# Kernel tuning notes

Hardware: AMD Instinct MI355X
Metric: run time of the kernel (lower is better)

The kernel has to match this reference:

```python
import jax, jax.numpy as jnp
import numpy as np

NUM_HEADS = 12

def setup_inputs() -> dict:
    key = jax.random.key(0)
    k1, k2, k3 = jax.random.split(key, 3)
    B, T, C = 1, 4096, 768
    x = jax.random.normal(k1, (B, T, C), dtype=jnp.float32)
    w_qkv = jax.random.normal(k2, (3 * C, C), dtype=jnp.float32) * (1.0 / np.sqrt(C))
    w_proj = jax.random.normal(k3, (C, C), dtype=jnp.float32) * (1.0 / np.sqrt(C))
    attn_mask = jnp.tril(jnp.ones((T, T), dtype=bool))  # causal block mask
    return {"x": x, "w_qkv": w_qkv, "w_proj": w_proj, "attn_mask": attn_mask}


def reference(x, w_qkv, w_proj, attn_mask):
    B, T, C = x.shape
    H = NUM_HEADS
    Dh = C // H
    # fused QKV projection (torch Linear: y = x @ W.T), then split
    qkv = jnp.einsum('btc,fc->btf', x, w_qkv)  # [B,T,3C]
    q, k, v = jnp.split(qkv, 3, axis=-1)
    # [B,T,C] -> [B,H,T,Dh]
    q = q.reshape(B, T, H, Dh).transpose(0, 2, 1, 3)
    k = k.reshape(B, T, H, Dh).transpose(0, 2, 1, 3)
    v = v.reshape(B, T, H, Dh).transpose(0, 2, 1, 3)
    # masked SDPA, default flex_attention scale = 1/sqrt(head_dim)
    scores = jnp.einsum('bhqd,bhkd->bhqk', q, k) * (1.0 / np.sqrt(Dh))
    neg = jnp.finfo(scores.dtype).min
    scores = jnp.where(attn_mask[None, None, :, :], scores, neg)
    attn = jax.nn.softmax(scores, axis=-1)
    y = jnp.einsum('bhqk,bhkd->bhqd', attn, v)
    # [B,H,T,Dh] -> [B,T,C], then output projection (dropout=0)
    y = y.transpose(0, 2, 1, 3).reshape(B, T, C)
    y = jnp.einsum('btc,fc->btf', y, w_proj)
    return y
```

## Files before the change

### kernel.cpp

```cpp
#include <hip/hip_runtime.h>

typedef unsigned short u16;
typedef unsigned int u32;
typedef __attribute__((ext_vector_type(8))) short s16x8;
typedef __attribute__((ext_vector_type(4))) float f32x4;
typedef __attribute__((ext_vector_type(4))) u16 u16x4;
typedef __attribute__((ext_vector_type(4))) u32 u32x4;

#define LOG2E 1.4426950408889634f

#if __has_builtin(__builtin_amdgcn_exp2f)
#define EXP2F __builtin_amdgcn_exp2f
#else
#define EXP2F exp2f
#endif

__device__ __forceinline__ u16 f32_to_bf16(float f) {
  union { float f; u32 u; } c; c.f = f;
  return (u16)((c.u + 0x7fffu + ((c.u >> 16) & 1u)) >> 16);
}

__device__ __forceinline__ u32 cvtpk(float lo, float hi) {
  u32 r;
  asm("v_cvt_pk_bf16_f32 %0, %1, %2" : "=v"(r) : "v"(lo), "v"(hi));
  return r;
}

__device__ __forceinline__ void async16(const void* g, void* l) {
  __builtin_amdgcn_global_load_lds(
      (__attribute__((address_space(1))) void*)g,
      (__attribute__((address_space(3))) void*)l, 16, 0, 0);
}

__global__ __launch_bounds__(256) void cast3_f32_bf16(const float* __restrict__ a,
                                                      const float* __restrict__ b,
                                                      const float* __restrict__ c,
                                                      u16* __restrict__ out,
                                                      int n1, int n2, int n3) {
  int i = (blockIdx.x * 256 + threadIdx.x) * 4;
  const float* src;
  int off = i;
  if (i < n1) {
    src = a;
  } else if (i < n1 + n2) {
    src = b; off = i - n1;
  } else if (i < n1 + n2 + n3) {
    src = c; off = i - n1 - n2;
  } else {
    return;
  }
  f32x4 v = *(const f32x4*)(src + off);
  u16x4 o;
  o[0] = f32_to_bf16(v[0]);
  o[1] = f32_to_bf16(v[1]);
  o[2] = f32_to_bf16(v[2]);
  o[3] = f32_to_bf16(v[3]);
  *(u16x4*)(out + i) = o;
}

__device__ __forceinline__ int vt_perm_inv(int k) {
  return (k & 35) | ((k & 16) >> 2) | ((k & 12) << 1);
}

__global__ __launch_bounds__(512) void qkv_gemm(const u16* __restrict__ A,
                                                const u16* __restrict__ B,
                                                u16* __restrict__ qk,
                                                u16* __restrict__ vt) {
  constexpr int K = 768;
  constexpr int BK = 32;
  constexpr int NT = K / BK;
  __shared__ alignas(16) u16 As[2][128 * BK];
  __shared__ alignas(16) u16 Bs[2][128 * BK];
  const int tid = threadIdx.x;
  const int lane = tid & 63;
  const int wid = tid >> 6;
  const int brow = blockIdx.x * 128;
  const int bcol = blockIdx.y * 128;
  const int wr = wid >> 2, wc = wid & 3;
  const int l15 = lane & 15, l4 = lane >> 4;
  f32x4 acc[4][2] = {};
  const int r0 = tid >> 2, s0 = tid & 3;

#define G1_STAGE(kt, b)                                                         \
  {                                                                             \
    async16(A + (size_t)(brow + r0) * K + (kt) * BK + s0 * 8, &As[b][tid * 8]); \
    async16(B + (size_t)(bcol + r0) * K + (kt) * BK + s0 * 8, &Bs[b][tid * 8]); \
  }

  G1_STAGE(0, 0);
  __syncthreads();
  int cur = 0;
  for (int kt = 0; kt < NT; ++kt) {
    if (kt + 1 < NT) G1_STAGE(kt + 1, cur ^ 1);
    s16x8 af[4], bf[2];
#pragma unroll
    for (int m = 0; m < 4; ++m)
      af[m] = *(const s16x8*)&As[cur][(wr * 64 + m * 16 + l15) * BK + l4 * 8];
#pragma unroll
    for (int n = 0; n < 2; ++n)
      bf[n] = *(const s16x8*)&Bs[cur][(wc * 32 + n * 16 + l15) * BK + l4 * 8];
#pragma unroll
    for (int m = 0; m < 4; ++m)
#pragma unroll
      for (int n = 0; n < 2; ++n)
        acc[m][n] = __builtin_amdgcn_mfma_f32_16x16x32_bf16(af[m], bf[n], acc[m][n], 0, 0, 0);
    __syncthreads();
    cur ^= 1;
  }
#undef G1_STAGE

  const int row0 = brow + wr * 64 + l4 * 4;
  const int col0 = bcol + wc * 32 + l15;
  if (bcol >= 1536) {
#pragma unroll
    for (int m = 0; m < 4; ++m) {
      int t0 = row0 + m * 16;
      int s = (t0 & ~63) + vt_perm_inv(t0 & 63);
#pragma unroll
      for (int n = 0; n < 2; ++n) {
        int vcol = col0 + n * 16 - 1536;
        u16x4 pk;
#pragma unroll
        for (int r = 0; r < 4; ++r) pk[r] = f32_to_bf16(acc[m][n][r]);
        *(u16x4*)&vt[(size_t)vcol * 4096 + s] = pk;
      }
    }
  } else {
    const float qs = (bcol < 768) ? 0.125f * LOG2E : 1.0f;
#pragma unroll
    for (int m = 0; m < 4; ++m)
#pragma unroll
      for (int n = 0; n < 2; ++n)
#pragma unroll
        for (int r = 0; r < 4; ++r)
          qk[(size_t)(row0 + m * 16 + r) * 1536 + (col0 + n * 16)] =
              f32_to_bf16(acc[m][n][r] * qs);
  }
}

__global__ __launch_bounds__(512) void proj_gemm(const u16* __restrict__ A,
                                                 const u16* __restrict__ B,
                                                 float* __restrict__ C) {
  constexpr int K = 768;
  constexpr int N = 768;
  constexpr int BK = 32;
  constexpr int NT = K / BK;
  __shared__ alignas(16) u16 As[2][128 * BK];
  __shared__ alignas(16) u16 Bs[2][128 * BK];
  const int tid = threadIdx.x;
  const int lane = tid & 63;
  const int wid = tid >> 6;
  const int brow = blockIdx.x * 128;
  const int bcol = blockIdx.y * 128;
  const int wr = wid >> 2, wc = wid & 3;
  const int l15 = lane & 15, l4 = lane >> 4;
  f32x4 acc[4][2] = {};
  const int r0 = tid >> 2, s0 = tid & 3;

#define G2_STAGE(kt, b)                                                         \
  {                                                                             \
    async16(A + (size_t)(brow + r0) * K + (kt) * BK + s0 * 8, &As[b][tid * 8]); \
    async16(B + (size_t)(bcol + r0) * K + (kt) * BK + s0 * 8, &Bs[b][tid * 8]); \
  }

  G2_STAGE(0, 0);
  __syncthreads();
  int cur = 0;
  for (int kt = 0; kt < NT; ++kt) {
    if (kt + 1 < NT) G2_STAGE(kt + 1, cur ^ 1);
    s16x8 af[4], bf[2];
#pragma unroll
    for (int m = 0; m < 4; ++m)
      af[m] = *(const s16x8*)&As[cur][(wr * 64 + m * 16 + l15) * BK + l4 * 8];
#pragma unroll
    for (int n = 0; n < 2; ++n)
      bf[n] = *(const s16x8*)&Bs[cur][(wc * 32 + n * 16 + l15) * BK + l4 * 8];
#pragma unroll
    for (int m = 0; m < 4; ++m)
#pragma unroll
      for (int n = 0; n < 2; ++n)
        acc[m][n] = __builtin_amdgcn_mfma_f32_16x16x32_bf16(af[m], bf[n], acc[m][n], 0, 0, 0);
    __syncthreads();
    cur ^= 1;
  }
#undef G2_STAGE

  const int row0 = brow + wr * 64 + l4 * 4;
  const int col0 = bcol + wc * 32 + l15;
#pragma unroll
  for (int m = 0; m < 4; ++m)
#pragma unroll
    for (int n = 0; n < 2; ++n)
#pragma unroll
      for (int r = 0; r < 4; ++r)
        C[(size_t)(row0 + m * 16 + r) * N + (col0 + n * 16)] = acc[m][n][r];
}

constexpr int cph_for(int C) {
  int s = 0;
  for (int qb = 0; qb < 32; ++qb) s += (2 * qb + 2 + C - 1) / C;
  return s;
}

template <int C>
__global__ __launch_bounds__(256) void attn_kernel(const u16* __restrict__ qk,
                                                   const u16* __restrict__ vt,
                                                   u16* __restrict__ y,
                                                   float* __restrict__ po,
                                                   float* __restrict__ pl) {
  constexpr int MAXCH = (64 + C - 1) / C;
  constexpr int CPH = cph_for(C);
  __shared__ alignas(16) u16 Ks[2][64 * 64];
  __shared__ alignas(16) u16 Vs[2][64 * 64];
  const int tid = threadIdx.x;
  const int lane = tid & 63;
  const int wid = tid >> 6;
  const int l15 = lane & 15, l4 = lane >> 4;

  const int h = blockIdx.x % 12;
  int c = CPH - 1 - (int)(blockIdx.x / 12);
  int qb = 0, ch = c;
  for (;;) {
    int n = (2 * qb + 2 + C - 1) / C;
    if (ch < n) break;
    ch -= n;
    ++qb;
  }
  const int NTt = 2 * qb + 2;
  const int nch = (NTt + C - 1) / C;

  const int qw0 = qb * 128 + wid * 32;

  s16x8 bq[2][2];
#pragma unroll
  for (int qf = 0; qf < 2; ++qf)
#pragma unroll
    for (int ks = 0; ks < 2; ++ks)
      bq[qf][ks] = *(const s16x8*)&qk[(size_t)(qw0 + qf * 16 + l15) * 1536 +
                                      h * 64 + ks * 32 + l4 * 8];

  f32x4 o[2][4] = {};
  f32x4 lacc[2] = {};

  const u16* Kb = qk + 768 + h * 64;
  const u16* Vb = vt + (size_t)(h * 64) * 4096;

  const int sc0 = tid, sc1 = tid + 256;
  const int sr0 = sc0 >> 3, sp0 = sc0 & 7;
  const int sr1 = sc1 >> 3, sp1 = sc1 & 7;

#define STAGE_KV(t, b)                                                                        \
  {                                                                                           \
    async16(Kb + (size_t)((t) * 64 + sr0) * 1536 + ((sp0 ^ (sr0 & 7)) * 8), &Ks[b][sc0 * 8]); \
    async16(Kb + (size_t)((t) * 64 + sr1) * 1536 + ((sp1 ^ (sr1 & 7)) * 8), &Ks[b][sc1 * 8]); \
    async16(Vb + (size_t)sr0 * 4096 + (t) * 64 + ((sp0 ^ (sr0 & 7)) * 8), &Vs[b][sc0 * 8]);   \
    async16(Vb + (size_t)sr1 * 4096 + (t) * 64 + ((sp1 ^ (sr1 & 7)) * 8), &Vs[b][sc1 * 8]);   \
  }

  const int t0 = ch * C;
  const int t1 = (t0 + C < NTt) ? t0 + C : NTt;
  STAGE_KV(t0, 0);
  __syncthreads();
  int cur = 0;
  for (int kt = t0; kt < t1; ++kt) {
    if (kt + 1 < t1) STAGE_KV(kt + 1, cur ^ 1);

    f32x4 s4[2][4];
    __builtin_amdgcn_s_setprio(1);
#pragma unroll
    for (int kf = 0; kf < 4; ++kf) {
      int r = kf * 16 + l15;
      s16x8 k0 = *(const s16x8*)&Ks[cur][r * 64 + ((l4 ^ (r & 7)) * 8)];
      s16x8 k1 = *(const s16x8*)&Ks[cur][r * 64 + (((l4 + 4) ^ (r & 7)) * 8)];
#pragma unroll
      for (int qf = 0; qf < 2; ++qf) {
        f32x4 a = {};
        a = __builtin_amdgcn_mfma_f32_16x16x32_bf16(k0, bq[qf][0], a, 0, 0, 0);
        a = __builtin_amdgcn_mfma_f32_16x16x32_bf16(k1, bq[qf][1], a, 0, 0, 0);
        s4[qf][kf] = a;
      }
    }
    __builtin_amdgcn_s_setprio(0);
    if (kt >= 2 * qb) {
#pragma unroll
      for (int qf = 0; qf < 2; ++qf) {
        int qg = qw0 + qf * 16 + l15;
#pragma unroll
        for (int kf = 0; kf < 4; ++kf)
#pragma unroll
          for (int r = 0; r < 4; ++r)
            if (kt * 64 + kf * 16 + l4 * 4 + r > qg) s4[qf][kf][r] = -1e30f;
      }
    }
    u32 w[2][4][2];
#pragma unroll
    for (int qf = 0; qf < 2; ++qf)
#pragma unroll
      for (int kf = 0; kf < 4; ++kf) {
        f32x4 p;
#pragma unroll
        for (int r = 0; r < 4; ++r) p[r] = EXP2F(s4[qf][kf][r]);
        lacc[qf] += p;
        w[qf][kf][0] = cvtpk(p[0], p[1]);
        w[qf][kf][1] = cvtpk(p[2], p[3]);
      }
    __builtin_amdgcn_s_setprio(1);
#pragma unroll
    for (int ks2 = 0; ks2 < 2; ++ks2) {
      s16x8 bp[2];
#pragma unroll
      for (int qf = 0; qf < 2; ++qf) {
        u32x4 bu;
        bu[0] = w[qf][2 * ks2][0];
        bu[1] = w[qf][2 * ks2][1];
        bu[2] = w[qf][2 * ks2 + 1][0];
        bu[3] = w[qf][2 * ks2 + 1][1];
        bp[qf] = __builtin_bit_cast(s16x8, bu);
      }
#pragma unroll
      for (int df = 0; df < 4; ++df) {
        int d = df * 16 + l15;
        int e = ks2 * 4 + l4;
        s16x8 av = *(const s16x8*)&Vs[cur][d * 64 + ((e ^ (d & 7)) * 8)];
#pragma unroll
        for (int qf = 0; qf < 2; ++qf)
          o[qf][df] = __builtin_amdgcn_mfma_f32_16x16x32_bf16(av, bp[qf], o[qf][df], 0, 0, 0);
      }
    }
    __builtin_amdgcn_s_setprio(0);
    __syncthreads();
    cur ^= 1;
  }
#undef STAGE_KV

  float lsum[2];
#pragma unroll
  for (int qf = 0; qf < 2; ++qf) {
    float s = lacc[qf][0] + lacc[qf][1] + lacc[qf][2] + lacc[qf][3];
    s += __shfl_xor(s, 16);
    s += __shfl_xor(s, 32);
    lsum[qf] = s;
  }

  if (nch == 1) {
#pragma unroll
    for (int qf = 0; qf < 2; ++qf) {
      float inv = 1.0f / lsum[qf];
#pragma unroll
      for (int df = 0; df < 4; ++df) {
        u16x4 pk;
#pragma unroll
        for (int r = 0; r < 4; ++r) pk[r] = f32_to_bf16(o[qf][df][r] * inv);
        *(u16x4*)&y[(size_t)(qw0 + qf * 16 + l15) * 768 + h * 64 + df * 16 + l4 * 4] = pk;
      }
    }
  } else {
    const size_t slot = (size_t)(h * 32 + qb) * MAXCH + ch;
#pragma unroll
    for (int qf = 0; qf < 2; ++qf) {
      float* ob = po + slot * 8192 + (size_t)(wid * 32 + qf * 16 + l15) * 64;
#pragma unroll
      for (int df = 0; df < 4; ++df)
        *(f32x4*)(ob + df * 16 + l4 * 4) = o[qf][df];
      if (lane < 16) pl[slot * 128 + wid * 32 + qf * 16 + l15] = lsum[qf];
    }
  }
}

template <int C>
__global__ __launch_bounds__(256) void attn_combine(const float* __restrict__ po,
                                                    const float* __restrict__ pl,
                                                    u16* __restrict__ y) {
  constexpr int MAXCH = (64 + C - 1) / C;
  const int h = blockIdx.x;
  const int qb = C / 2 + blockIdx.y;
  const int nch = (2 * qb + 2 + C - 1) / C;
  const int tid = threadIdx.x;
  const int q = tid >> 1;
  const int d0 = (tid & 1) * 32;

  f32x4 acc[8] = {};
  float lt = 0.f;
  for (int s = 0; s < nch; ++s) {
    const size_t slot = (size_t)(h * 32 + qb) * MAXCH + s;
    lt += pl[slot * 128 + q];
    const float* ob = po + slot * 8192 + (size_t)q * 64 + d0;
#pragma unroll
    for (int j = 0; j < 8; ++j) acc[j] += *(const f32x4*)(ob + j * 4);
  }
  float inv = 1.0f / lt;
  u16* yp = &y[(size_t)(qb * 128 + q) * 768 + h * 64 + d0];
#pragma unroll
  for (int j = 0; j < 8; ++j) {
    u16x4 pk;
#pragma unroll
    for (int r = 0; r < 4; ++r) pk[r] = f32_to_bf16(acc[j][r] * inv);
    *(u16x4*)(yp + j * 4) = pk;
  }
}

extern "C" void kernel_launch(void* const* d_in, const int* in_sizes, int n_in,
                              void* d_out, int out_size, void* d_ws, size_t ws_size,
                              hipStream_t stream) {
  const float* x = (const float*)d_in[0];
  const float* w_qkv = (const float*)d_in[1];
  const float* w_proj = (const float*)d_in[2];
  float* out = (float*)d_out;

  u16* ws = (u16*)d_ws;
  u16* xb = ws;
  u16* wqkvb = xb + 4096 * 768;
  u16* wprojb = wqkvb + 2304 * 768;
  u16* qkb = wprojb + 768 * 768;
  u16* vtb = qkb + (size_t)4096 * 1536;
  u16* yb = vtb + (size_t)768 * 4096;
  const size_t base_u16 = (size_t)4096 * 768 + 2304 * 768 + 768 * 768 +
                          (size_t)4096 * 1536 + (size_t)768 * 4096 + (size_t)4096 * 768;
  float* pf = (float*)(ws + base_u16);
  const size_t base_b = base_u16 * 2;

  constexpr int N1 = 4096 * 768, N2 = 2304 * 768, N3 = 768 * 768;
  cast3_f32_bf16<<<(N1 + N2 + N3) / 4 / 256, 256, 0, stream>>>(
      x, w_qkv, w_proj, xb, N1, N2, N3);

  qkv_gemm<<<dim3(32, 18), 512, 0, stream>>>(xb, wqkvb, qkb, vtb);

  const size_t need8 = base_b + (size_t)(12 * 32 * 8) * (8192 + 128) * 4;
  const size_t need16 = base_b + (size_t)(12 * 32 * 4) * (8192 + 128) * 4;
  const size_t need32 = base_b + (size_t)(12 * 32 * 2) * (8192 + 128) * 4;
  if (ws_size >= need8) {
    constexpr int C = 8, MAXCH = 8;
    float* po = pf;
    float* pl = po + (size_t)12 * 32 * MAXCH * 8192;
    attn_kernel<C><<<12 * cph_for(C), 256, 0, stream>>>(qkb, vtb, yb, po, pl);
    attn_combine<C><<<dim3(12, 32 - C / 2), 256, 0, stream>>>(po, pl, yb);
  } else if (ws_size >= need16) {
    constexpr int C = 16, MAXCH = 4;
    float* po = pf;
    float* pl = po + (size_t)12 * 32 * MAXCH * 8192;
    attn_kernel<C><<<12 * cph_for(C), 256, 0, stream>>>(qkb, vtb, yb, po, pl);
    attn_combine<C><<<dim3(12, 32 - C / 2), 256, 0, stream>>>(po, pl, yb);
  } else if (ws_size >= need32) {
    constexpr int C = 32, MAXCH = 2;
    float* po = pf;
    float* pl = po + (size_t)12 * 32 * MAXCH * 8192;
    attn_kernel<C><<<12 * cph_for(C), 256, 0, stream>>>(qkb, vtb, yb, po, pl);
    attn_combine<C><<<dim3(12, 32 - C / 2), 256, 0, stream>>>(po, pl, yb);
  } else {
    constexpr int C = 64;
    attn_kernel<C><<<12 * cph_for(C), 256, 0, stream>>>(qkb, vtb, yb, nullptr, nullptr);
  }

  proj_gemm<<<dim3(32, 6), 512, 0, stream>>>(yb, wprojb, out);
}
```

Baseline: 114.3 us.

## Retile QKV and projection GEMMs and balance attention KV split chunks

Doubles the QKV GEMM K-tile to 64, adding an XOR swizzle on LDS to avoid bank conflicts. Shrinks the projection GEMM to 64x64 tiles with 256 threads so more blocks cover the device. Replaces the fixed-size attention KV chunking with a target-based even split, so chunk counts scale with each query block's causal length and the combine pass skips unsplit blocks. These aim to raise occupancy and balance work, at the cost of more LDS per block in the QKV GEMM and extra combine launches.

```diff
diff --git a/kernel.cpp b/kernel.cpp
--- a/kernel.cpp
+++ b/kernel.cpp
@@ -67,7 +67,7 @@
                                                 u16* __restrict__ qk,
                                                 u16* __restrict__ vt) {
   constexpr int K = 768;
-  constexpr int BK = 32;
+  constexpr int BK = 64;
   constexpr int NT = K / BK;
   __shared__ alignas(16) u16 As[2][128 * BK];
   __shared__ alignas(16) u16 Bs[2][128 * BK];
@@ -79,12 +79,16 @@
   const int wr = wid >> 2, wc = wid & 3;
   const int l15 = lane & 15, l4 = lane >> 4;
   f32x4 acc[4][2] = {};
-  const int r0 = tid >> 2, s0 = tid & 3;
-
-#define G1_STAGE(kt, b)                                                         \
-  {                                                                             \
-    async16(A + (size_t)(brow + r0) * K + (kt) * BK + s0 * 8, &As[b][tid * 8]); \
-    async16(B + (size_t)(bcol + r0) * K + (kt) * BK + s0 * 8, &Bs[b][tid * 8]); \
+  const int c0 = tid, c1 = tid + 512;
+  const int r0 = c0 >> 3, p0 = c0 & 7;
+  const int r1 = c1 >> 3, p1 = c1 & 7;
+
+#define G1_STAGE(kt, b)                                                                       \
+  {                                                                                           \
+    async16(A + (size_t)(brow + r0) * K + (kt) * BK + ((p0 ^ (r0 & 7)) * 8), &As[b][c0 * 8]); \
+    async16(A + (size_t)(brow + r1) * K + (kt) * BK + ((p1 ^ (r1 & 7)) * 8), &As[b][c1 * 8]); \
+    async16(B + (size_t)(bcol + r0) * K + (kt) * BK + ((p0 ^ (r0 & 7)) * 8), &Bs[b][c0 * 8]); \
+    async16(B + (size_t)(bcol + r1) * K + (kt) * BK + ((p1 ^ (r1 & 7)) * 8), &Bs[b][c1 * 8]); \
   }
 
   G1_STAGE(0, 0);
@@ -92,18 +96,27 @@
   int cur = 0;
   for (int kt = 0; kt < NT; ++kt) {
     if (kt + 1 < NT) G1_STAGE(kt + 1, cur ^ 1);
-    s16x8 af[4], bf[2];
+    s16x8 af[2][4], bf[2][2];
+#pragma unroll
+    for (int kk = 0; kk < 2; ++kk) {
+#pragma unroll
+      for (int m = 0; m < 4; ++m) {
+        int r = wr * 64 + m * 16 + l15;
+        af[kk][m] = *(const s16x8*)&As[cur][r * BK + (((kk * 4 + l4) ^ (r & 7)) * 8)];
+      }
+#pragma unroll
+      for (int n = 0; n < 2; ++n) {
+        int r = wc * 32 + n * 16 + l15;
+        bf[kk][n] = *(const s16x8*)&Bs[cur][r * BK + (((kk * 4 + l4) ^ (r & 7)) * 8)];
+      }
+    }
 #pragma unroll
     for (int m = 0; m < 4; ++m)
-      af[m] = *(const s16x8*)&As[cur][(wr * 64 + m * 16 + l15) * BK + l4 * 8];
-#pragma unroll
-    for (int n = 0; n < 2; ++n)
-      bf[n] = *(const s16x8*)&Bs[cur][(wc * 32 + n * 16 + l15) * BK + l4 * 8];
-#pragma unroll
-    for (int m = 0; m < 4; ++m)
-#pragma unroll
-      for (int n = 0; n < 2; ++n)
-        acc[m][n] = __builtin_amdgcn_mfma_f32_16x16x32_bf16(af[m], bf[n], acc[m][n], 0, 0, 0);
+#pragma unroll
+      for (int n = 0; n < 2; ++n) {
+        acc[m][n] = __builtin_amdgcn_mfma_f32_16x16x32_bf16(af[0][m], bf[0][n], acc[m][n], 0, 0, 0);
+        acc[m][n] = __builtin_amdgcn_mfma_f32_16x16x32_bf16(af[1][m], bf[1][n], acc[m][n], 0, 0, 0);
+      }
     __syncthreads();
     cur ^= 1;
   }
@@ -138,23 +151,23 @@
   }
 }
 
-__global__ __launch_bounds__(512) void proj_gemm(const u16* __restrict__ A,
+__global__ __launch_bounds__(256) void proj_gemm(const u16* __restrict__ A,
                                                  const u16* __restrict__ B,
                                                  float* __restrict__ C) {
   constexpr int K = 768;
   constexpr int N = 768;
   constexpr int BK = 32;
   constexpr int NT = K / BK;
-  __shared__ alignas(16) u16 As[2][128 * BK];
-  __shared__ alignas(16) u16 Bs[2][128 * BK];
+  __shared__ alignas(16) u16 As[2][64 * BK];
+  __shared__ alignas(16) u16 Bs[2][64 * BK];
   const int tid = threadIdx.x;
   const int lane = tid & 63;
   const int wid = tid >> 6;
-  const int brow = blockIdx.x * 128;
-  const int bcol = blockIdx.y * 128;
-  const int wr = wid >> 2, wc = wid & 3;
+  const int brow = blockIdx.x * 64;
+  const int bcol = blockIdx.y * 64;
+  const int wr = wid >> 1, wc = wid & 1;
   const int l15 = lane & 15, l4 = lane >> 4;
-  f32x4 acc[4][2] = {};
+  f32x4 acc[2][2] = {};
   const int r0 = tid >> 2, s0 = tid & 3;
 
 #define G2_STAGE(kt, b)                                                         \
@@ -168,15 +181,15 @@
   int cur = 0;
   for (int kt = 0; kt < NT; ++kt) {
     if (kt + 1 < NT) G2_STAGE(kt + 1, cur ^ 1);
-    s16x8 af[4], bf[2];
-#pragma unroll
-    for (int m = 0; m < 4; ++m)
-      af[m] = *(const s16x8*)&As[cur][(wr * 64 + m * 16 + l15) * BK + l4 * 8];
+    s16x8 af[2], bf[2];
+#pragma unroll
+    for (int m = 0; m < 2; ++m)
+      af[m] = *(const s16x8*)&As[cur][(wr * 32 + m * 16 + l15) * BK + l4 * 8];
 #pragma unroll
     for (int n = 0; n < 2; ++n)
       bf[n] = *(const s16x8*)&Bs[cur][(wc * 32 + n * 16 + l15) * BK + l4 * 8];
 #pragma unroll
-    for (int m = 0; m < 4; ++m)
+    for (int m = 0; m < 2; ++m)
 #pragma unroll
       for (int n = 0; n < 2; ++n)
         acc[m][n] = __builtin_amdgcn_mfma_f32_16x16x32_bf16(af[m], bf[n], acc[m][n], 0, 0, 0);
@@ -185,10 +198,10 @@
   }
 #undef G2_STAGE
 
-  const int row0 = brow + wr * 64 + l4 * 4;
+  const int row0 = brow + wr * 32 + l4 * 4;
   const int col0 = bcol + wc * 32 + l15;
 #pragma unroll
-  for (int m = 0; m < 4; ++m)
+  for (int m = 0; m < 2; ++m)
 #pragma unroll
     for (int n = 0; n < 2; ++n)
 #pragma unroll
@@ -196,20 +209,23 @@
         C[(size_t)(row0 + m * 16 + r) * N + (col0 + n * 16)] = acc[m][n][r];
 }
 
-constexpr int cph_for(int C) {
+__host__ __device__ constexpr int nch_for(int qb, int TGT) {
+  int n = (2 * qb + 2 + TGT / 2 - 1) / TGT;
+  return n < 1 ? 1 : n;
+}
+__host__ __device__ constexpr int cph_for(int TGT) {
   int s = 0;
-  for (int qb = 0; qb < 32; ++qb) s += (2 * qb + 2 + C - 1) / C;
+  for (int qb = 0; qb < 32; ++qb) s += nch_for(qb, TGT);
   return s;
 }
 
-template <int C>
+template <int TGT, int MAXCH>
 __global__ __launch_bounds__(256) void attn_kernel(const u16* __restrict__ qk,
                                                    const u16* __restrict__ vt,
                                                    u16* __restrict__ y,
                                                    float* __restrict__ po,
                                                    float* __restrict__ pl) {
-  constexpr int MAXCH = (64 + C - 1) / C;
-  constexpr int CPH = cph_for(C);
+  constexpr int CPH = cph_for(TGT);
   __shared__ alignas(16) u16 Ks[2][64 * 64];
   __shared__ alignas(16) u16 Vs[2][64 * 64];
   const int tid = threadIdx.x;
@@ -221,13 +237,13 @@
   int c = CPH - 1 - (int)(blockIdx.x / 12);
   int qb = 0, ch = c;
   for (;;) {
-    int n = (2 * qb + 2 + C - 1) / C;
+    int n = nch_for(qb, TGT);
     if (ch < n) break;
     ch -= n;
     ++qb;
   }
   const int NTt = 2 * qb + 2;
-  const int nch = (NTt + C - 1) / C;
+  const int nch = nch_for(qb, TGT);
 
   const int qw0 = qb * 128 + wid * 32;
 
@@ -257,8 +273,8 @@
     async16(Vb + (size_t)sr1 * 4096 + (t) * 64 + ((sp1 ^ (sr1 & 7)) * 8), &Vs[b][sc1 * 8]);   \
   }
 
-  const int t0 = ch * C;
-  const int t1 = (t0 + C < NTt) ? t0 + C : NTt;
+  const int t0 = ch * NTt / nch;
+  const int t1 = (ch + 1) * NTt / nch;
   STAGE_KV(t0, 0);
   __syncthreads();
   int cur = 0;
@@ -367,14 +383,14 @@
   }
 }
 
-template <int C>
+template <int TGT, int MAXCH>
 __global__ __launch_bounds__(256) void attn_combine(const float* __restrict__ po,
                                                     const float* __restrict__ pl,
                                                     u16* __restrict__ y) {
-  constexpr int MAXCH = (64 + C - 1) / C;
   const int h = blockIdx.x;
-  const int qb = C / 2 + blockIdx.y;
-  const int nch = (2 * qb + 2 + C - 1) / C;
+  const int qb = blockIdx.y;
+  const int nch = nch_for(qb, TGT);
+  if (nch == 1) return;
   const int tid = threadIdx.x;
   const int q = tid >> 1;
   const int d0 = (tid & 1) * 32;
@@ -425,31 +441,17 @@
 
   qkv_gemm<<<dim3(32, 18), 512, 0, stream>>>(xb, wqkvb, qkb, vtb);
 
-  const size_t need8 = base_b + (size_t)(12 * 32 * 8) * (8192 + 128) * 4;
-  const size_t need16 = base_b + (size_t)(12 * 32 * 4) * (8192 + 128) * 4;
-  const size_t need32 = base_b + (size_t)(12 * 32 * 2) * (8192 + 128) * 4;
-  if (ws_size >= need8) {
-    constexpr int C = 8, MAXCH = 8;
+  constexpr int TGT = 12;
+  constexpr int MAXCH = nch_for(31, TGT);
+  const size_t need = base_b + (size_t)(12 * 32 * MAXCH) * (8192 + 128) * 4;
+  if (ws_size >= need) {
     float* po = pf;
     float* pl = po + (size_t)12 * 32 * MAXCH * 8192;
-    attn_kernel<C><<<12 * cph_for(C), 256, 0, stream>>>(qkb, vtb, yb, po, pl);
-    attn_combine<C><<<dim3(12, 32 - C / 2), 256, 0, stream>>>(po, pl, yb);
-  } else if (ws_size >= need16) {
-    constexpr int C = 16, MAXCH = 4;
-    float* po = pf;
-    float* pl = po + (size_t)12 * 32 * MAXCH * 8192;
-    attn_kernel<C><<<12 * cph_for(C), 256, 0, stream>>>(qkb, vtb, yb, po, pl);
-    attn_combine<C><<<dim3(12, 32 - C / 2), 256, 0, stream>>>(po, pl, yb);
-  } else if (ws_size >= need32) {
-    constexpr int C = 32, MAXCH = 2;
-    float* po = pf;
-    float* pl = po + (size_t)12 * 32 * MAXCH * 8192;
-    attn_kernel<C><<<12 * cph_for(C), 256, 0, stream>>>(qkb, vtb, yb, po, pl);
-    attn_combine<C><<<dim3(12, 32 - C / 2), 256, 0, stream>>>(po, pl, yb);
+    attn_kernel<TGT, MAXCH><<<12 * cph_for(TGT), 256, 0, stream>>>(qkb, vtb, yb, po, pl);
+    attn_combine<TGT, MAXCH><<<dim3(12, 32), 256, 0, stream>>>(po, pl, yb);
   } else {
-    constexpr int C = 64;
-    attn_kernel<C><<<12 * cph_for(C), 256, 0, stream>>>(qkb, vtb, yb, nullptr, nullptr);
-  }
-
-  proj_gemm<<<dim3(32, 6), 512, 0, stream>>>(yb, wprojb, out);
-}
+    attn_kernel<1000, 1><<<12 * cph_for(1000), 256, 0, stream>>>(qkb, vtb, yb, nullptr, nullptr);
+  }
+
+  proj_gemm<<<dim3(64, 12), 256, 0, stream>>>(yb, wprojb, out);
+}
```

Result: no change. 114.3 us (+0.0%).

## Shrink proj tiles, single-buffer attention KV, compute row sums via MFMA

Applied to the files above, without the earlier changes.

The projection GEMM moves to 64x64 tiles with 256 threads and a 64x12 grid, giving more blocks for the CUs. The attention kernel drops KV double buffering in favour of one LDS buffer with two barriers per tile. This cuts LDS use and may allow more blocks per CU, but it loses the overlap of loads with compute. Softmax row sums are now computed with an extra MFMA against a ones vector instead of VALU adds and shuffles. The combine launch covers all query blocks and returns early for single-chunk ones.

```diff
diff --git a/kernel.cpp b/kernel.cpp
--- a/kernel.cpp
+++ b/kernel.cpp
@@ -138,23 +138,23 @@
   }
 }
 
-__global__ __launch_bounds__(512) void proj_gemm(const u16* __restrict__ A,
+__global__ __launch_bounds__(256) void proj_gemm(const u16* __restrict__ A,
                                                  const u16* __restrict__ B,
                                                  float* __restrict__ C) {
   constexpr int K = 768;
   constexpr int N = 768;
   constexpr int BK = 32;
   constexpr int NT = K / BK;
-  __shared__ alignas(16) u16 As[2][128 * BK];
-  __shared__ alignas(16) u16 Bs[2][128 * BK];
+  __shared__ alignas(16) u16 As[2][64 * BK];
+  __shared__ alignas(16) u16 Bs[2][64 * BK];
   const int tid = threadIdx.x;
   const int lane = tid & 63;
   const int wid = tid >> 6;
-  const int brow = blockIdx.x * 128;
-  const int bcol = blockIdx.y * 128;
-  const int wr = wid >> 2, wc = wid & 3;
+  const int brow = blockIdx.x * 64;
+  const int bcol = blockIdx.y * 64;
+  const int wr = wid >> 1, wc = wid & 1;
   const int l15 = lane & 15, l4 = lane >> 4;
-  f32x4 acc[4][2] = {};
+  f32x4 acc[2][2] = {};
   const int r0 = tid >> 2, s0 = tid & 3;
 
 #define G2_STAGE(kt, b)                                                         \
@@ -168,15 +168,15 @@
   int cur = 0;
   for (int kt = 0; kt < NT; ++kt) {
     if (kt + 1 < NT) G2_STAGE(kt + 1, cur ^ 1);
-    s16x8 af[4], bf[2];
-#pragma unroll
-    for (int m = 0; m < 4; ++m)
-      af[m] = *(const s16x8*)&As[cur][(wr * 64 + m * 16 + l15) * BK + l4 * 8];
+    s16x8 af[2], bf[2];
+#pragma unroll
+    for (int m = 0; m < 2; ++m)
+      af[m] = *(const s16x8*)&As[cur][(wr * 32 + m * 16 + l15) * BK + l4 * 8];
 #pragma unroll
     for (int n = 0; n < 2; ++n)
       bf[n] = *(const s16x8*)&Bs[cur][(wc * 32 + n * 16 + l15) * BK + l4 * 8];
 #pragma unroll
-    for (int m = 0; m < 4; ++m)
+    for (int m = 0; m < 2; ++m)
 #pragma unroll
       for (int n = 0; n < 2; ++n)
         acc[m][n] = __builtin_amdgcn_mfma_f32_16x16x32_bf16(af[m], bf[n], acc[m][n], 0, 0, 0);
@@ -185,10 +185,10 @@
   }
 #undef G2_STAGE
 
-  const int row0 = brow + wr * 64 + l4 * 4;
+  const int row0 = brow + wr * 32 + l4 * 4;
   const int col0 = bcol + wc * 32 + l15;
 #pragma unroll
-  for (int m = 0; m < 4; ++m)
+  for (int m = 0; m < 2; ++m)
 #pragma unroll
     for (int n = 0; n < 2; ++n)
 #pragma unroll
@@ -210,8 +210,8 @@
                                                    float* __restrict__ pl) {
   constexpr int MAXCH = (64 + C - 1) / C;
   constexpr int CPH = cph_for(C);
-  __shared__ alignas(16) u16 Ks[2][64 * 64];
-  __shared__ alignas(16) u16 Vs[2][64 * 64];
+  __shared__ alignas(16) u16 Ks[64 * 64];
+  __shared__ alignas(16) u16 Vs[64 * 64];
   const int tid = threadIdx.x;
   const int lane = tid & 63;
   const int wid = tid >> 6;
@@ -239,8 +239,11 @@
       bq[qf][ks] = *(const s16x8*)&qk[(size_t)(qw0 + qf * 16 + l15) * 1536 +
                                       h * 64 + ks * 32 + l4 * 8];
 
+  const short oval = (l15 == 0) ? (short)0x3F80 : (short)0;
+  const s16x8 aone = {oval, oval, oval, oval, oval, oval, oval, oval};
+
   f32x4 o[2][4] = {};
-  f32x4 lacc[2] = {};
+  f32x4 lv[2] = {};
 
   const u16* Kb = qk + 768 + h * 64;
   const u16* Vb = vt + (size_t)(h * 64) * 4096;
@@ -249,29 +252,28 @@
   const int sr0 = sc0 >> 3, sp0 = sc0 & 7;
   const int sr1 = sc1 >> 3, sp1 = sc1 & 7;
 
-#define STAGE_KV(t, b)                                                                        \
-  {                                                                                           \
-    async16(Kb + (size_t)((t) * 64 + sr0) * 1536 + ((sp0 ^ (sr0 & 7)) * 8), &Ks[b][sc0 * 8]); \
-    async16(Kb + (size_t)((t) * 64 + sr1) * 1536 + ((sp1 ^ (sr1 & 7)) * 8), &Ks[b][sc1 * 8]); \
-    async16(Vb + (size_t)sr0 * 4096 + (t) * 64 + ((sp0 ^ (sr0 & 7)) * 8), &Vs[b][sc0 * 8]);   \
-    async16(Vb + (size_t)sr1 * 4096 + (t) * 64 + ((sp1 ^ (sr1 & 7)) * 8), &Vs[b][sc1 * 8]);   \
+#define STAGE_KV(t)                                                                        \
+  {                                                                                        \
+    async16(Kb + (size_t)((t) * 64 + sr0) * 1536 + ((sp0 ^ (sr0 & 7)) * 8), &Ks[sc0 * 8]); \
+    async16(Kb + (size_t)((t) * 64 + sr1) * 1536 + ((sp1 ^ (sr1 & 7)) * 8), &Ks[sc1 * 8]); \
+    async16(Vb + (size_t)sr0 * 4096 + (t) * 64 + ((sp0 ^ (sr0 & 7)) * 8), &Vs[sc0 * 8]);   \
+    async16(Vb + (size_t)sr1 * 4096 + (t) * 64 + ((sp1 ^ (sr1 & 7)) * 8), &Vs[sc1 * 8]);   \
   }
 
   const int t0 = ch * C;
   const int t1 = (t0 + C < NTt) ? t0 + C : NTt;
-  STAGE_KV(t0, 0);
-  __syncthreads();
-  int cur = 0;
   for (int kt = t0; kt < t1; ++kt) {
-    if (kt + 1 < t1) STAGE_KV(kt + 1, cur ^ 1);
+    __syncthreads();
+    STAGE_KV(kt);
+    __syncthreads();
 
     f32x4 s4[2][4];
     __builtin_amdgcn_s_setprio(1);
 #pragma unroll
     for (int kf = 0; kf < 4; ++kf) {
       int r = kf * 16 + l15;
-      s16x8 k0 = *(const s16x8*)&Ks[cur][r * 64 + ((l4 ^ (r & 7)) * 8)];
-      s16x8 k1 = *(const s16x8*)&Ks[cur][r * 64 + (((l4 + 4) ^ (r & 7)) * 8)];
+      s16x8 k0 = *(const s16x8*)&Ks[r * 64 + ((l4 ^ (r & 7)) * 8)];
+      s16x8 k1 = *(const s16x8*)&Ks[r * 64 + (((l4 + 4) ^ (r & 7)) * 8)];
 #pragma unroll
       for (int qf = 0; qf < 2; ++qf) {
         f32x4 a = {};
@@ -300,7 +302,6 @@
         f32x4 p;
 #pragma unroll
         for (int r = 0; r < 4; ++r) p[r] = EXP2F(s4[qf][kf][r]);
-        lacc[qf] += p;
         w[qf][kf][0] = cvtpk(p[0], p[1]);
         w[qf][kf][1] = cvtpk(p[2], p[3]);
       }
@@ -321,26 +322,23 @@
       for (int df = 0; df < 4; ++df) {
         int d = df * 16 + l15;
         int e = ks2 * 4 + l4;
-        s16x8 av = *(const s16x8*)&Vs[cur][d * 64 + ((e ^ (d & 7)) * 8)];
+        s16x8 av = *(const s16x8*)&Vs[d * 64 + ((e ^ (d & 7)) * 8)];
 #pragma unroll
         for (int qf = 0; qf < 2; ++qf)
           o[qf][df] = __builtin_amdgcn_mfma_f32_16x16x32_bf16(av, bp[qf], o[qf][df], 0, 0, 0);
       }
+#pragma unroll
+      for (int qf = 0; qf < 2; ++qf)
+        lv[qf] = __builtin_amdgcn_mfma_f32_16x16x32_bf16(aone, bp[qf], lv[qf], 0, 0, 0);
     }
     __builtin_amdgcn_s_setprio(0);
-    __syncthreads();
-    cur ^= 1;
   }
 #undef STAGE_KV
 
   float lsum[2];
 #pragma unroll
-  for (int qf = 0; qf < 2; ++qf) {
-    float s = lacc[qf][0] + lacc[qf][1] + lacc[qf][2] + lacc[qf][3];
-    s += __shfl_xor(s, 16);
-    s += __shfl_xor(s, 32);
-    lsum[qf] = s;
-  }
+  for (int qf = 0; qf < 2; ++qf)
+    lsum[qf] = __shfl(lv[qf][0], l15);
 
   if (nch == 1) {
 #pragma unroll
@@ -373,8 +371,9 @@
                                                     u16* __restrict__ y) {
   constexpr int MAXCH = (64 + C - 1) / C;
   const int h = blockIdx.x;
-  const int qb = C / 2 + blockIdx.y;
+  const int qb = blockIdx.y;
   const int nch = (2 * qb + 2 + C - 1) / C;
+  if (nch == 1) return;
   const int tid = threadIdx.x;
   const int q = tid >> 1;
   const int d0 = (tid & 1) * 32;
@@ -433,23 +432,23 @@
     float* po = pf;
     float* pl = po + (size_t)12 * 32 * MAXCH * 8192;
     attn_kernel<C><<<12 * cph_for(C), 256, 0, stream>>>(qkb, vtb, yb, po, pl);
-    attn_combine<C><<<dim3(12, 32 - C / 2), 256, 0, stream>>>(po, pl, yb);
+    attn_combine<C><<<dim3(12, 32), 256, 0, stream>>>(po, pl, yb);
   } else if (ws_size >= need16) {
     constexpr int C = 16, MAXCH = 4;
     float* po = pf;
     float* pl = po + (size_t)12 * 32 * MAXCH * 8192;
     attn_kernel<C><<<12 * cph_for(C), 256, 0, stream>>>(qkb, vtb, yb, po, pl);
-    attn_combine<C><<<dim3(12, 32 - C / 2), 256, 0, stream>>>(po, pl, yb);
+    attn_combine<C><<<dim3(12, 32), 256, 0, stream>>>(po, pl, yb);
   } else if (ws_size >= need32) {
     constexpr int C = 32, MAXCH = 2;
     float* po = pf;
     float* pl = po + (size_t)12 * 32 * MAXCH * 8192;
     attn_kernel<C><<<12 * cph_for(C), 256, 0, stream>>>(qkb, vtb, yb, po, pl);
-    attn_combine<C><<<dim3(12, 32 - C / 2), 256, 0, stream>>>(po, pl, yb);
+    attn_combine<C><<<dim3(12, 32), 256, 0, stream>>>(po, pl, yb);
   } else {
     constexpr int C = 64;
     attn_kernel<C><<<12 * cph_for(C), 256, 0, stream>>>(qkb, vtb, yb, nullptr, nullptr);
   }
 
-  proj_gemm<<<dim3(32, 6), 512, 0, stream>>>(yb, wprojb, out);
-}
+  proj_gemm<<<dim3(64, 12), 256, 0, stream>>>(yb, wprojb, out);
+}
```

Result: slower. 116.7 us (+2.1%).
